# Optimization experiments

Measured on AMD Instinct MI355X. Metric: run time of the kernel, lower is better.

## Reference

```python
import jax, jax.numpy as jnp
import numpy as np

B, DIM, H, W = 4, 96, 256, 256
HEADS = 4
EPS = 1e-12

def conv1x1(x, w, b):
    # x: [b,c,h,w], w: [o,c,1,1], b: [o]
    return jnp.einsum('bchw,oc->bohw', x, w[:, :, 0, 0]) + b[None, :, None, None]

def dwconv3x3(x, w, b):
    # depthwise 3x3, w: [c,1,3,3]
    c = x.shape[1]
    y = jax.lax.conv_general_dilated(
        x, w, window_strides=(1, 1), padding='SAME',
        feature_group_count=c, dimension_numbers=('NCHW', 'OIHW', 'NCHW'))
    return y + b[None, :, None, None]

def setup_inputs() -> dict:
    key = jax.random.key(0)
    ks = jax.random.split(key, 16)
    d = DIM
    s = 0.05
    return {
        'content': jax.random.normal(ks[0], (B, d, H, W), jnp.float32),
        'style': jax.random.normal(ks[1], (B, d, H, W), jnp.float32),
        'temperature': jnp.ones((HEADS, 1, 1), jnp.float32),
        'q_w': jax.random.normal(ks[2], (d, d, 1, 1), jnp.float32) * s,
        'q_b': jax.random.normal(ks[3], (d,), jnp.float32) * s,
        'qd_w': jax.random.normal(ks[4], (d, 1, 3, 3), jnp.float32) * s,
        'qd_b': jax.random.normal(ks[5], (d,), jnp.float32) * s,
        'kv_w': jax.random.normal(ks[6], (3 * d, d, 1, 1), jnp.float32) * s,
        'kv_b': jax.random.normal(ks[7], (3 * d,), jnp.float32) * s,
        'kvd_w': jax.random.normal(ks[8], (3 * d, 1, 3, 3), jnp.float32) * s,
        'kvd_b': jax.random.normal(ks[9], (3 * d,), jnp.float32) * s,
        'ps_w': jax.random.normal(ks[10], (d, d, 1, 1), jnp.float32) * s,
        'ps_b': jax.random.normal(ks[11], (d,), jnp.float32) * s,
        'psh_w': jax.random.normal(ks[12], (d, d, 1, 1), jnp.float32) * s,
        'psh_b': jax.random.normal(ks[13], (d,), jnp.float32) * s,
    }

def _heads(x, b, h, w):
    # [b, head*c, h, w] -> [b, head, c, h*w]
    return x.reshape(b, HEADS, x.shape[1] // HEADS, h * w)

def reference(content, style, temperature, q_w, q_b, qd_w, qd_b,
              kv_w, kv_b, kvd_w, kvd_b, ps_w, ps_b, psh_w, psh_b):
    b, c, h, w = content.shape
    kv = dwconv3x3(conv1x1(style, kv_w, kv_b), kvd_w, kvd_b)
    k, v_scale, v_shift = jnp.split(kv, 3, axis=1)
    q = dwconv3x3(conv1x1(content, q_w, q_b), qd_w, qd_b)

    q = _heads(q, b, h, w)
    k = _heads(k, b, h, w)
    v_scale = _heads(v_scale, b, h, w)
    v_shift = _heads(v_shift, b, h, w)

    # L2-normalize over spatial dim (torch F.normalize eps=1e-12)
    q = q / jnp.maximum(jnp.linalg.norm(q, axis=-1, keepdims=True), EPS)
    k = k / jnp.maximum(jnp.linalg.norm(k, axis=-1, keepdims=True), EPS)

    # attn: [b, head, c, c] (channel attention, tiny)
    attn = jnp.einsum('bhcn,bhdn->bhcd', q, k) * temperature[None]
    attn = jax.nn.softmax(attn, axis=-1)

    scale = jnp.einsum('bhcd,bhdn->bhcn', attn, v_scale).reshape(b, c, h, w)
    shift = jnp.einsum('bhcd,bhdn->bhcn', attn, v_shift).reshape(b, c, h, w)

    scale = conv1x1(scale, ps_w, ps_b)
    shift = conv1x1(shift, psh_w, psh_b)
    return (scale, shift)
```

## Files before the change

kernel.cpp:

```cpp
#include <hip/hip_runtime.h>

#define NB 4
#define C 96
#define HH 256
#define WW 256
#define NPIX (HH*WW)
#define HEADS 4
#define CH 24

#define NTX2 16
#define NTY2 19
#define NTILES (NTX2*NTY2)
#define YP 296
#define QP 264
#define VP 104
#define KSPLIT 128
#define YR 24
#define YC 392
#define XTP 76
#define VCH 40

#define WS_SUMSQ_Q 0
#define WS_SUMSQ_K (WS_SUMSQ_Q + NB*C)
#define WS_GRAM    (WS_SUMSQ_K + NB*C)
#define WS_MS      (WS_GRAM + NB*HEADS*CH*CH)
#define WS_MSH     (WS_MS + NB*C*C)

#define XT_OFF_BYTES ((size_t)335872)
#define XT_BYTES   ((size_t)2*NB*NPIX*96*2)

#define F_PSQ_OFF   (XT_OFF_BYTES + XT_BYTES)
#define F_PSQ_BYTES ((size_t)NTILES*NB*192*4)
#define F_PG_OFF    (F_PSQ_OFF + F_PSQ_BYTES)
#define F_PG_BYTES  ((size_t)NTILES*NB*HEADS*1024*4)
#define F_MB_OFF    (F_PG_OFF + F_PG_BYTES)
#define F_MB_BYTES  ((size_t)2*NB*96*96*2)
#define F_WS_NEED   (F_MB_OFF + F_MB_BYTES)

#define QK_OFF    (XT_OFF_BYTES + XT_BYTES)
#define QK_BYTES  ((size_t)2*NB*96*NPIX*2)
#define PG_OFF    (QK_OFF + QK_BYTES)
#define PG_BYTES  ((size_t)KSPLIT*NB*9216*4)
#define PSQ_OFF   (PG_OFF + PG_BYTES)
#define PSQ_BYTES ((size_t)4*NTILES*NB*48*4)
#define MB_OFF    (PSQ_OFF + PSQ_BYTES)
#define MB_BYTES  ((size_t)2*NB*96*96*2)
#define WB_OFF    (MB_OFF + MB_BYTES)
#define WB_BYTES  ((size_t)384*96*2)
#define WS_NEED3  (WB_OFF + WB_BYTES)

typedef short short8 __attribute__((ext_vector_type(8)));
typedef float f32x4 __attribute__((ext_vector_type(4)));
typedef float f32x16 __attribute__((ext_vector_type(16)));

__device__ __forceinline__ unsigned short f2b(float f){
  unsigned u = __float_as_uint(f);
  unsigned r = u + 0x7FFFu + ((u >> 16) & 1u);
  return (unsigned short)(r >> 16);
}
__device__ __forceinline__ float b2f(unsigned short s){
  return __uint_as_float(((unsigned)s) << 16);
}
__device__ __forceinline__ unsigned cvtpk(float lo, float hi){
  unsigned r;
  asm("v_cvt_pk_bf16_f32 %0, %1, %2" : "=v"(r) : "v"(lo), "v"(hi));
  return r;
}
__device__ __forceinline__ short8 pack8(float4 a, float4 b){
  short8 r;
  r[0]=(short)f2b(a.x); r[1]=(short)f2b(a.y); r[2]=(short)f2b(a.z); r[3]=(short)f2b(a.w);
  r[4]=(short)f2b(b.x); r[5]=(short)f2b(b.y); r[6]=(short)f2b(b.z); r[7]=(short)f2b(b.w);
  return r;
}

__global__ __launch_bounds__(256) void k0t(
  const float* __restrict__ content, const float* __restrict__ style,
  unsigned short* __restrict__ xt, int cm)
{
  __shared__ unsigned short Xt[96*XTP];
  const int t = threadIdx.x;
  const int n0 = blockIdx.x * 64;
  const int b = blockIdx.y, src = blockIdx.z;
  const int gyr = n0 >> 8, gxb = n0 & 255;
  const float* in = (src ? style : content) + (size_t)b*C*NPIX;
  #pragma unroll
  for (int i = 0; i < 6; ++i){
    int s = i*256 + t;
    int r = s >> 4, c4 = s & 15;
    float4 f = *(const float4*)(in + (size_t)r*NPIX + n0 + c4*4);
    unsigned lo = ((unsigned)f2b(f.y) << 16) | f2b(f.x);
    unsigned hi = ((unsigned)f2b(f.w) << 16) | f2b(f.z);
    *(uint2*)&Xt[r*XTP + c4*4] = make_uint2(lo, hi);
  }
  __syncthreads();
  unsigned* dst = (unsigned*)(xt + ((size_t)src*NB + b)*NPIX*96);
  #pragma unroll
  for (int i = 0; i < 12; ++i){
    int s = i*256 + t;
    int j = s / 48, c2 = s - j*48;
    unsigned v = ((unsigned)Xt[(c2*2+1)*XTP + j] << 16) | Xt[(c2*2)*XTP + j];
    size_t np = cm ? ((size_t)(gxb + j)*HH + gyr) : (size_t)(n0 + j);
    dst[np*48 + c2] = v;
  }
}

__global__ __launch_bounds__(256) void kwpack(
  const float* __restrict__ q_w, const float* __restrict__ kv_w,
  unsigned short* __restrict__ wb)
{
  int i = blockIdx.x*256 + threadIdx.x;
  if (i < 9216) wb[i] = f2b(q_w[i]);
  else if (i < 36864) wb[i] = f2b(kv_w[i - 9216]);
}

__global__ __launch_bounds__(512, 4) void kconv(
  const unsigned short* __restrict__ xt, const unsigned short* __restrict__ wb,
  const float* __restrict__ q_b, const float* __restrict__ qd_w, const float* __restrict__ qd_b,
  const float* __restrict__ kv_b, const float* __restrict__ kvd_w, const float* __restrict__ kvd_b,
  unsigned short* __restrict__ qk, float* __restrict__ psq)
{
  __shared__ unsigned short Ysh[48*YC];
  __shared__ float red[48];
  const int t = threadIdx.x, lane = t & 63, w = t >> 6;
  const int tile = blockIdx.x, b = blockIdx.y, z = blockIdx.z;
  const int txx = tile & 15, tyy = tile >> 4;
  const int gx0 = txx*16, gy0 = tyy*14;
  const unsigned short* xsrc = xt + ((size_t)((z < 2 ? 0 : 1)*NB + b))*NPIX*96;
  const int wrow0 = (z < 2) ? z*48 : 96 + (z-2)*48;
  const float* cb  = (z<2) ? q_b  + z*48           : kv_b  + (size_t)(z-2)*48;
  const float* dww = (z<2) ? qd_w + (size_t)z*48*9 : kvd_w + (size_t)(z-2)*48*9;
  const float* dwb = (z<2) ? qd_b + z*48           : kvd_b + (size_t)(z-2)*48;
  unsigned short* dst0 = (z < 2)
      ? qk + ((size_t)(0*NB + b)*96 + (size_t)z*48)*NPIX
      : qk + ((size_t)(1*NB + b)*96 + (size_t)(z-2)*48)*NPIX;

  if (t < 48) red[t] = 0.f;

  const int hy = lane & 15, khalf = lane >> 4;
  const int gyh = gy0 - 1 + hy;
  short8 xf[3][3]; bool imv[3];
  const int np = (w < 2) ? 3 : 2;
  #pragma unroll
  for (int i = 0; i < 3; ++i){
    if (i >= np) break;
    int pt = w + i*8;
    int gx = gx0 - 1 + pt;
    bool im = (gx>=0) && (gx<WW) && (gyh>=0) && (gyh<HH);
    imv[i] = im;
    const unsigned short* xp = xsrc + (size_t)(im ? (gx*HH + gyh) : 0)*96 + khalf*8;
    short8 zz = {};
    #pragma unroll
    for (int kk = 0; kk < 3; ++kk){
      short8 v = *(const short8*)(xp + kk*32);
      xf[i][kk] = im ? v : zz;
    }
  }

  #pragma unroll 1
  for (int mi = 0; mi < 3; ++mi){
    const unsigned short* wp = wb + (size_t)(wrow0 + mi*16 + hy)*96 + khalf*8;
    short8 a0 = *(const short8*)(wp);
    short8 a1 = *(const short8*)(wp + 32);
    short8 a2 = *(const short8*)(wp + 64);
    float4 bv = *(const float4*)&cb[mi*16 + khalf*4];
    #pragma unroll
    for (int i = 0; i < 3; ++i){
      if (i >= np) break;
      int pt = w + i*8;
      f32x4 acc = {bv.x, bv.y, bv.z, bv.w};
      acc = __builtin_amdgcn_mfma_f32_16x16x32_bf16(a0, xf[i][0], acc, 0,0,0);
      acc = __builtin_amdgcn_mfma_f32_16x16x32_bf16(a1, xf[i][1], acc, 0,0,0);
      acc = __builtin_amdgcn_mfma_f32_16x16x32_bf16(a2, xf[i][2], acc, 0,0,0);
      #pragma unroll
      for (int r = 0; r < 4; ++r){
        int ch = mi*16 + khalf*4 + r;
        Ysh[ch*YC + hy*YR + pt] = imv[i] ? f2b(acc[r]) : (unsigned short)0;
      }
    }
  }
  __syncthreads();

  for (int sl = lane; sl < 84; sl += 64){
    int slot = w*84 + sl;
    int c = slot / 14, py = slot - (slot/14)*14;
    int gy = gy0 + py;
    if (gy < HH){
      const float* wd = dww + (size_t)c*9;
      float w00=wd[0],w01=wd[1],w02=wd[2],w10=wd[3],w11=wd[4],w12=wd[5],w20=wd[6],w21=wd[7],w22=wd[8];
      float bb = dwb[c];
      const unsigned short* yb = &Ysh[c*YC + py*YR];
      float o[16];
      #pragma unroll
      for (int half = 0; half < 2; ++half){
        float u[3][10];
        #pragma unroll
        for (int uu = 0; uu < 3; ++uu){
          const unsigned short* rp = yb + uu*YR + half*8;
          short8 s = *(const short8*)rp;
          unsigned ex = *(const unsigned*)(rp + 8);
          #pragma unroll
          for (int j = 0; j < 8; ++j) u[uu][j] = b2f((unsigned short)s[j]);
          u[uu][8] = b2f((unsigned short)(ex & 0xffffu));
          u[uu][9] = b2f((unsigned short)(ex >> 16));
        }
        #pragma unroll
        for (int j = 0; j < 8; ++j){
          float s = bb;
          s = fmaf(w00,u[0][j],s); s = fmaf(w01,u[0][j+1],s); s = fmaf(w02,u[0][j+2],s);
          s = fmaf(w10,u[1][j],s); s = fmaf(w11,u[1][j+1],s); s = fmaf(w12,u[1][j+2],s);
          s = fmaf(w20,u[2][j],s); s = fmaf(w21,u[2][j+1],s); s = fmaf(w22,u[2][j+2],s);
          o[half*8 + j] = s;
        }
      }
      float sq = 0.f;
      #pragma unroll
      for (int j = 0; j < 16; ++j) sq = fmaf(o[j], o[j], sq);
      atomicAdd(&red[c], sq);
      unsigned vvp[8];
      #pragma unroll
      for (int jj = 0; jj < 8; ++jj) vvp[jj] = cvtpk(o[2*jj], o[2*jj+1]);
      unsigned short* qp = dst0 + (size_t)c*NPIX + (size_t)gy*WW + gx0;
      *(uint4*)qp       = make_uint4(vvp[0], vvp[1], vvp[2], vvp[3]);
      *(uint4*)(qp + 8) = make_uint4(vvp[4], vvp[5], vvp[6], vvp[7]);
    }
  }
  __syncthreads();
  if (t < 48)
    psq[((size_t)(z*NTILES + tile)*NB + b)*48 + t] = red[t];
}

__global__ __launch_bounds__(384) void kgram(
  const unsigned short* __restrict__ qk, float* __restrict__ pg)
{
  const int t = threadIdx.x, lane = t & 63, wv = t >> 6;
  const int ks = blockIdx.x, b = blockIdx.y;
  const int n0 = ks * (NPIX / KSPLIT);
  const unsigned short* qb = qk + ((size_t)(0*NB + b)*96)*NPIX;
  const unsigned short* kb = qk + ((size_t)(1*NB + b)*96)*NPIX;
  f32x4 acc[6];
  #pragma unroll
  for (int i = 0; i < 6; ++i) acc[i] = (f32x4){0.f,0.f,0.f,0.f};
  #pragma unroll 1
  for (int st = 0; st < (NPIX/KSPLIT)/32; ++st){
    int off = n0 + st*32 + (lane>>4)*8;
    short8 bf = *(const short8*)(kb + (size_t)(wv*16 + (lane&15))*NPIX + off);
    #pragma unroll
    for (int ci = 0; ci < 6; ++ci){
      short8 af = *(const short8*)(qb + (size_t)(ci*16 + (lane&15))*NPIX + off);
      acc[ci] = __builtin_amdgcn_mfma_f32_16x16x32_bf16(af, bf, acc[ci], 0,0,0);
    }
  }
  float* dst = pg + ((size_t)ks*NB + b)*9216;
  #pragma unroll
  for (int ci = 0; ci < 6; ++ci){
    #pragma unroll
    for (int r = 0; r < 4; ++r)
      dst[(ci*6 + wv)*256 + ((lane>>4)*4 + r)*16 + (lane&15)] = acc[ci][r];
  }
}

__global__ __launch_bounds__(256) void kgredN(
  const float* __restrict__ pg, const float* __restrict__ psq, float* __restrict__ ws)
{
  const int b = blockIdx.x, by = blockIdx.y, t = threadIdx.x;
  if (by < 36){
    int ci = by / 6;
    int qrow = ci*16 + (t >> 4), krow = (by - ci*6)*16 + (t & 15);
    float s = 0.f;
    for (int ks = 0; ks < KSPLIT; ++ks)
      s += pg[((size_t)ks*NB + b)*9216 + by*256 + t];
    int h = qrow / CH;
    if (krow / CH == h)
      ws[WS_GRAM + ((size_t)(b*HEADS + h)*CH + (qrow % CH))*CH + (krow % CH)] = s;
  } else {
    if (t < 192){
      int src = t / 96, c = t - (t/96)*96;
      int zz = src*2 + (c/48), cc = c - (c/48)*48;
      float s = 0.f;
      for (int tile = 0; tile < NTILES; ++tile)
        s += psq[((size_t)(zz*NTILES + tile)*NB + b)*48 + cc];
      ws[(src ? WS_SUMSQ_K : WS_SUMSQ_Q) + b*C + c] = s;
    }
  }
}

__global__ void k2_attn(
  const float* __restrict__ temp,
  const float* __restrict__ ps_w, const float* __restrict__ psh_w,
  float* __restrict__ ws, unsigned short* __restrict__ mb)
{
  const int b = blockIdx.x;
  const int t = threadIdx.x;
  __shared__ float attn[C * CH];
  __shared__ float nq[C], nk[C];
  if (t < C){
    nq[t] = fmaxf(sqrtf(ws[WS_SUMSQ_Q + b * C + t]), 1e-12f);
    nk[t] = fmaxf(sqrtf(ws[WS_SUMSQ_K + b * C + t]), 1e-12f);
  }
  __syncthreads();
  if (t < C){
    int h = t / CH;
    const float* g = ws + WS_GRAM + (((size_t)b * HEADS + h) * CH + (t % CH)) * CH;
    float tp = temp[h];
    float row[CH];
    float mx = -3.4e38f;
    #pragma unroll
    for (int d = 0; d < CH; ++d){
      row[d] = g[d] / (nq[t] * nk[h * CH + d]) * tp;
      mx = fmaxf(mx, row[d]);
    }
    float s = 0.f;
    #pragma unroll
    for (int d = 0; d < CH; ++d){ row[d] = expf(row[d] - mx); s += row[d]; }
    float inv = 1.f / s;
    #pragma unroll
    for (int d = 0; d < CH; ++d) attn[t * CH + d] = row[d] * inv;
  }
  __syncthreads();
  for (int idx = t; idx < C * C; idx += 256){
    int o = idx / C, dg = idx - o * C;
    int h = dg / CH, d = dg - h * CH;
    float s1 = 0.f, s2 = 0.f;
    #pragma unroll
    for (int c2 = 0; c2 < CH; ++c2){
      float a = attn[(h * CH + c2) * CH + d];
      s1 = fmaf(ps_w [(size_t)o * C + h * CH + c2], a, s1);
      s2 = fmaf(psh_w[(size_t)o * C + h * CH + c2], a, s2);
    }
    ws[WS_MS  + (size_t)b * C * C + idx] = s1;
    ws[WS_MSH + (size_t)b * C * C + idx] = s2;
    if (mb){
      mb[((size_t)0*NB + b)*9216 + idx] = f2b(s1);
      mb[((size_t)1*NB + b)*9216 + idx] = f2b(s2);
    }
  }
}

__global__ __launch_bounds__(512, 4) void kvm(
  const unsigned short* __restrict__ xt, const unsigned short* __restrict__ wb,
  const float* __restrict__ kv_b, const float* __restrict__ kvd_w, const float* __restrict__ kvd_b,
  const unsigned short* __restrict__ mb,
  const float* __restrict__ ps_b, const float* __restrict__ psh_b,
  float* __restrict__ out)
{
  __shared__ unsigned short Ysh[32*YC];
  __shared__ unsigned short vS[224*VCH];
  const int t = threadIdx.x, lane = t & 63, w = t >> 6;
  const int tile = blockIdx.x, b = blockIdx.y, z = blockIdx.z;
  const int txx = tile & 15, tyy = tile >> 4;
  const int gx0 = txx*16, gy0 = tyy*14;
  const unsigned short* xsrc = xt + ((size_t)(NB + b))*NPIX*96;

  const int hy = lane & 15, khalf = lane >> 4;
  const int gyh = gy0 - 1 + hy;
  short8 xf[3][3]; bool imv[3];
  const int np = (w < 2) ? 3 : 2;
  #pragma unroll
  for (int i = 0; i < 3; ++i){
    if (i >= np) break;
    int pt = w + i*8;
    int gx = gx0 - 1 + pt;
    bool im = (gx>=0) && (gx<WW) && (gyh>=0) && (gyh<HH);
    imv[i] = im;
    const unsigned short* xp = xsrc + (size_t)(im ? (gx*HH + gyh) : 0)*96 + khalf*8;
    short8 zz = {};
    #pragma unroll
    for (int kk = 0; kk < 3; ++kk){
      short8 v = *(const short8*)(xp + kk*32);
      xf[i][kk] = im ? v : zz;
    }
  }

  const float* bias = z ? psh_b : ps_b;
  f32x4 acc[6][2];
  #pragma unroll
  for (int mi = 0; mi < 6; ++mi){
    float4 bv = *(const float4*)&bias[mi*16 + khalf*4];
    acc[mi][0] = (f32x4){bv.x, bv.y, bv.z, bv.w};
    acc[mi][1] = acc[mi][0];
  }
  const unsigned short* mbp = mb + ((size_t)z*NB + b)*9216;

  #pragma unroll 1
  for (int ck = 0; ck < 3; ++ck){
    const int kvrow0 = 96 + z*96 + ck*32;
    #pragma unroll 1
    for (int mi2 = 0; mi2 < 2; ++mi2){
      const unsigned short* wp = wb + (size_t)(96 + kvrow0 + mi2*16 + hy)*96 + khalf*8;
      short8 a0 = *(const short8*)(wp);
      short8 a1 = *(const short8*)(wp + 32);
      short8 a2 = *(const short8*)(wp + 64);
      float4 bv = *(const float4*)&kv_b[kvrow0 + mi2*16 + khalf*4];
      #pragma unroll
      for (int i = 0; i < 3; ++i){
        if (i >= np) break;
        int pt = w + i*8;
        f32x4 a = {bv.x, bv.y, bv.z, bv.w};
        a = __builtin_amdgcn_mfma_f32_16x16x32_bf16(a0, xf[i][0], a, 0,0,0);
        a = __builtin_amdgcn_mfma_f32_16x16x32_bf16(a1, xf[i][1], a, 0,0,0);
        a = __builtin_amdgcn_mfma_f32_16x16x32_bf16(a2, xf[i][2], a, 0,0,0);
        #pragma unroll
        for (int r = 0; r < 4; ++r){
          int ch = mi2*16 + khalf*4 + r;
          Ysh[ch*YC + hy*YR + pt] = imv[i] ? f2b(a[r]) : (unsigned short)0;
        }
      }
    }
    __syncthreads();
    if (t < 448){
      int c2 = t & 31, py = t >> 5;
      const float* wd = kvd_w + (size_t)(kvrow0 + c2)*9;
      float w00=wd[0],w01=wd[1],w02=wd[2],w10=wd[3],w11=wd[4],w12=wd[5],w20=wd[6],w21=wd[7],w22=wd[8];
      float bb = kvd_b[kvrow0 + c2];
      const unsigned short* yb = &Ysh[c2*YC + py*YR];
      float o[16];
      #pragma unroll
      for (int half = 0; half < 2; ++half){
        float u[3][10];
        #pragma unroll
        for (int uu = 0; uu < 3; ++uu){
          const unsigned short* rp = yb + uu*YR + half*8;
          short8 s = *(const short8*)rp;
          unsigned ex = *(const unsigned*)(rp + 8);
          #pragma unroll
          for (int j = 0; j < 8; ++j) u[uu][j] = b2f((unsigned short)s[j]);
          u[uu][8] = b2f((unsigned short)(ex & 0xffffu));
          u[uu][9] = b2f((unsigned short)(ex >> 16));
        }
        #pragma unroll
        for (int j = 0; j < 8; ++j){
          float s = bb;
          s = fmaf(w00,u[0][j],s); s = fmaf(w01,u[0][j+1],s); s = fmaf(w02,u[0][j+2],s);
          s = fmaf(w10,u[1][j],s); s = fmaf(w11,u[1][j+1],s); s = fmaf(w12,u[1][j+2],s);
          s = fmaf(w20,u[2][j],s); s = fmaf(w21,u[2][j+1],s); s = fmaf(w22,u[2][j+2],s);
          o[half*8 + j] = s;
        }
      }
      #pragma unroll
      for (int jj = 0; jj < 8; ++jj){
        unsigned p = cvtpk(o[2*jj], o[2*jj+1]);
        vS[(py*16 + 2*jj    )*VCH + c2] = (unsigned short)p;
        vS[(py*16 + 2*jj + 1)*VCH + c2] = (unsigned short)(p >> 16);
      }
    }
    __syncthreads();
    #pragma unroll
    for (int mi = 0; mi < 6; ++mi){
      short8 a = *(const short8*)(mbp + (size_t)(mi*16 + hy)*96 + ck*32 + khalf*8);
      #pragma unroll
      for (int gi = 0; gi < 2; ++gi){
        int g = w + gi*8;
        if (g < 14){
          short8 bf = *(const short8*)&vS[(size_t)(g*16 + hy)*VCH + khalf*8];
          acc[mi][gi] = __builtin_amdgcn_mfma_f32_16x16x32_bf16(a, bf, acc[mi][gi], 0,0,0);
        }
      }
    }
    __syncthreads();
  }

  float* ob = out + ((size_t)z*NB + b)*(size_t)C*NPIX;
  #pragma unroll
  for (int gi = 0; gi < 2; ++gi){
    int g = w + gi*8;
    int gy = gy0 + g;
    if (g < 14 && gy < HH){
      #pragma unroll
      for (int mi = 0; mi < 6; ++mi){
        #pragma unroll
        for (int r = 0; r < 4; ++r)
          __builtin_nontemporal_store(acc[mi][gi][r],
            &ob[(size_t)(mi*16 + khalf*4 + r)*NPIX + (size_t)gy*WW + gx0 + hy]);
      }
    }
  }
}

__device__ __forceinline__ void conv48c(
  const unsigned short* __restrict__ xbase, const float* __restrict__ wmat,
  const float* __restrict__ bias, int row0,
  int gx0, int gy0, int lane, int w, unsigned short* __restrict__ Ysh)
{
  const int hy = lane & 15, khalf = lane >> 4;
  const int gy = gy0 - 1 + hy;
  short8 xf[3][3]; bool imv[3]; int np = (w < 2) ? 3 : 2;
  #pragma unroll
  for (int i = 0; i < 3; ++i){
    if (i >= np) break;
    int pt = w + i*8;
    int gx = gx0 - 1 + pt;
    bool im = (gx>=0) && (gx<WW) && (gy>=0) && (gy<HH);
    imv[i] = im;
    int n = im ? (gy*WW + gx) : 0;
    const unsigned short* xp = xbase + (size_t)n*96 + khalf*8;
    short8 z = {};
    #pragma unroll
    for (int kk = 0; kk < 3; ++kk){
      short8 v = *(const short8*)(xp + kk*32);
      xf[i][kk] = im ? v : z;
    }
  }
  #pragma unroll 1
  for (int mi = 0; mi < 3; ++mi){
    int orow = row0 + mi*16 + hy;
    const float* wp = wmat + (size_t)orow*96 + khalf*8;
    short8 a0 = pack8(*(const float4*)(wp),    *(const float4*)(wp+4));
    short8 a1 = pack8(*(const float4*)(wp+32), *(const float4*)(wp+36));
    short8 a2 = pack8(*(const float4*)(wp+64), *(const float4*)(wp+68));
    float4 bv = *(const float4*)&bias[row0 + mi*16 + khalf*4];
    #pragma unroll
    for (int i = 0; i < 3; ++i){
      if (i >= np) break;
      int pt = w + i*8;
      f32x4 acc = {bv.x, bv.y, bv.z, bv.w};
      acc = __builtin_amdgcn_mfma_f32_16x16x32_bf16(a0, xf[i][0], acc, 0,0,0);
      acc = __builtin_amdgcn_mfma_f32_16x16x32_bf16(a1, xf[i][1], acc, 0,0,0);
      acc = __builtin_amdgcn_mfma_f32_16x16x32_bf16(a2, xf[i][2], acc, 0,0,0);
      #pragma unroll
      for (int r = 0; r < 4; ++r){
        int ch = mi*16 + khalf*4 + r;
        Ysh[ch*YP + pt*16 + hy] = imv[i] ? f2b(acc[r]) : (unsigned short)0;
      }
    }
  }
}

__global__ __launch_bounds__(512, 4) void kqk(
  const unsigned short* __restrict__ xt,
  const float* __restrict__ q_w, const float* __restrict__ q_b,
  const float* __restrict__ qd_w, const float* __restrict__ qd_b,
  const float* __restrict__ kv_w, const float* __restrict__ kv_b,
  const float* __restrict__ kvd_w, const float* __restrict__ kvd_b,
  float* __restrict__ pg, float* __restrict__ psq)
{
  __shared__ unsigned short Ysh[48*YP];
  __shared__ unsigned short qS[48*QP];
  __shared__ unsigned short kT[48*QP];
  __shared__ float redq[C], redk[C];

  const int t = threadIdx.x, lane = t & 63, w = t >> 6;
  const int b = blockIdx.y, tile = blockIdx.x;
  const int txx = tile & 15, tyy = tile >> 4;
  const int gx0 = txx*16, gy0 = tyy*14;
  if (t < C){ redq[t] = 0.f; redk[t] = 0.f; }
  __syncthreads();

  const unsigned short* xc = xt + ((size_t)(0*NB + b))*NPIX*96;
  const unsigned short* xs = xt + ((size_t)(1*NB + b))*NPIX*96;

  auto dwQK = [&](const float* dww, const float* dwb, int wrow0,
                  unsigned short* dst, float* red){
    for (int slot = t; slot < 48*16; slot += 512){
      int c = slot >> 4, j = slot & 15;
      const unsigned short* yb = &Ysh[c*YP + j*16];
      float u0[16], u1[16], u2[16];
      {
        short8 s0 = *(const short8*)(yb);
        short8 s1 = *(const short8*)(yb+8);
        short8 s2 = *(const short8*)(yb+16), s3 = *(const short8*)(yb+24);
        short8 s4 = *(const short8*)(yb+32), s5 = *(const short8*)(yb+40);
        #pragma unroll
        for (int u = 0; u < 8; ++u){
          u0[u]=b2f((unsigned short)s0[u]); u0[u+8]=b2f((unsigned short)s1[u]);
          u1[u]=b2f((unsigned short)s2[u]); u1[u+8]=b2f((unsigned short)s3[u]);
          u2[u]=b2f((unsigned short)s4[u]); u2[u+8]=b2f((unsigned short)s5[u]);
        }
      }
      const float* wd = dww + (size_t)(wrow0 + c)*9;
      float w00=wd[0],w01=wd[1],w02=wd[2],w10=wd[3],w11=wd[4],w12=wd[5],w20=wd[6],w21=wd[7],w22=wd[8];
      float bb = dwb[wrow0 + c];
      unsigned short vv[16];
      float sq = 0.f;
      #pragma unroll
      for (int py = 0; py < 14; ++py){
        float s = bb;
        s = fmaf(w00,u0[py],s); s = fmaf(w10,u0[py+1],s); s = fmaf(w20,u0[py+2],s);
        s = fmaf(w01,u1[py],s); s = fmaf(w11,u1[py+1],s); s = fmaf(w21,u1[py+2],s);
        s = fmaf(w02,u2[py],s); s = fmaf(w12,u2[py+1],s); s = fmaf(w22,u2[py+2],s);
        if (gy0 + py >= HH) s = 0.f;
        sq = fmaf(s, s, sq);
        vv[py] = f2b(s);
      }
      vv[14] = 0; vv[15] = 0;
      atomicAdd(&red[wrow0 + c], sq);
      *(short8*)&dst[c*QP + j*16]     = *(short8*)&vv[0];
      *(short8*)&dst[c*QP + j*16 + 8] = *(short8*)&vv[8];
    }
  };

  auto gram = [&](int cc){
    int hl = w & 1, slice = w >> 1;
    int cl = lane & 31; bool cv = cl < CH;
    int row = hl*CH + (cv ? cl : 0);
    f32x16 g;
    #pragma unroll
    for (int r = 0; r < 16; ++r) g[r] = 0.f;
    short8 z = {};
    for (int ks = slice; ks < 16; ks += 4){
      int ko = ks*16 + (lane>>5)*8;
      short8 qa = *(const short8*)&qS[row*QP + ko];
      short8 kb = *(const short8*)&kT[row*QP + ko];
      if (!cv){ qa = z; kb = z; }
      g = __builtin_amdgcn_mfma_f32_32x32x16_bf16(qa, kb, g, 0,0,0);
    }
    float* stg = (float*)Ysh;
    if (slice != 0){
      float* dst = stg + (size_t)(hl*3 + slice - 1)*1024;
      #pragma unroll
      for (int r = 0; r < 16; ++r) dst[r*64 + lane] = g[r];
    }
    __syncthreads();
    if (slice == 0){
      const float* s0 = stg + (size_t)(hl*3 + 0)*1024;
      const float* s1 = stg + (size_t)(hl*3 + 1)*1024;
      const float* s2 = stg + (size_t)(hl*3 + 2)*1024;
      float* dst = pg + ((size_t)(tile*NB + b)*HEADS + cc*2 + hl)*1024;
      #pragma unroll
      for (int r = 0; r < 16; ++r){
        int ix = r*64 + lane;
        dst[ix] = g[r] + s0[ix] + s1[ix] + s2[ix];
      }
    }
  };

  #pragma unroll 1
  for (int cc = 0; cc < 2; ++cc){
    conv48c(xc, q_w, q_b, cc*48, gx0, gy0, lane, w, Ysh);
    __syncthreads();
    dwQK(qd_w, qd_b, cc*48, qS, redq);
    __syncthreads();
    conv48c(xs, kv_w, kv_b, cc*48, gx0, gy0, lane, w, Ysh);
    __syncthreads();
    dwQK(kvd_w, kvd_b, cc*48, kT, redk);
    __syncthreads();
    gram(cc);
    __syncthreads();
  }
  if (t < 192){
    float v = (t < 96) ? redq[t] : redk[t - 96];
    psq[(size_t)(tile*NB + b)*192 + t] = v;
  }
}

__global__ __launch_bounds__(256) void kgredF(
  const float* __restrict__ pg, const float* __restrict__ psq, float* __restrict__ ws)
{
  const int bh = blockIdx.x;
  const int b = bh >> 2, h = bh & 3;
  const int t = threadIdx.x;
  float a0=0.f, a1=0.f, a2=0.f, a3=0.f, sq=0.f;
  for (int tile = 0; tile < NTILES; ++tile){
    const float* p = pg + ((size_t)(tile*NB + b)*HEADS + h)*1024;
    a0 += p[t]; a1 += p[t+256]; a2 += p[t+512]; a3 += p[t+768];
    if (t < 48){
      int ch = h*CH + (t % CH);
      sq += psq[(size_t)(tile*NB + b)*192 + (t < CH ? ch : 96 + ch)];
    }
  }
  if (t < 48){
    if (t < CH) ws[WS_SUMSQ_Q + b*C + h*CH + t] = sq;
    else        ws[WS_SUMSQ_K + b*C + h*CH + (t - CH)] = sq;
  }
  float accs[4] = {a0, a1, a2, a3};
  #pragma unroll
  for (int i = 0; i < 4; ++i){
    int idx = i*256 + t;
    int r = idx >> 6, ln = idx & 63;
    int row = (r&3) + 8*(r>>2) + 4*(ln>>5);
    int col = ln & 31;
    if (row < CH && col < CH)
      ws[WS_GRAM + ((size_t)(b*HEADS + h)*CH + row)*CH + col] = accs[i];
  }
}

__global__ __launch_bounds__(512, 4) void kv_out(
  const unsigned short* __restrict__ xs,
  const float* __restrict__ kv_w, const float* __restrict__ kv_b,
  const float* __restrict__ kvd_w, const float* __restrict__ kvd_b,
  const float* __restrict__ ps_b, const float* __restrict__ psh_b,
  const unsigned short* __restrict__ mb, float* __restrict__ out)
{
  __shared__ unsigned short Ysh[48*YP];
  __shared__ unsigned short vS2[224*VP];
  const int t = threadIdx.x, lane = t & 63, w = t >> 6;
  const int b = blockIdx.y, tile = blockIdx.x;
  const int txx = tile & 15, tyy = tile >> 4;
  const int gx0 = txx*16, gy0 = tyy*14;
  const unsigned short* xb_ = xs + (size_t)b*NPIX*96;

  #pragma unroll 1
  for (int which = 0; which < 2; ++which){
    #pragma unroll 1
    for (int cv = 0; cv < 2; ++cv){
      int row0 = 96 + which*96 + cv*48;
      conv48c(xb_, kv_w, kv_b, row0, gx0, gy0, lane, w, Ysh);
      __syncthreads();
      for (int slot = t; slot < 48*16; slot += 512){
        int c = slot >> 4, j = slot & 15;
        const unsigned short* yb = &Ysh[c*YP + j*16];
        float u0[16], u1[16], u2[16];
        {
          short8 s0 = *(const short8*)(yb),    s1 = *(const short8*)(yb+8);
          short8 s2 = *(const short8*)(yb+16), s3 = *(const short8*)(yb+24);
          short8 s4 = *(const short8*)(yb+32), s5 = *(const short8*)(yb+40);
          #pragma unroll
          for (int u = 0; u < 8; ++u){
            u0[u]=b2f((unsigned short)s0[u]); u0[u+8]=b2f((unsigned short)s1[u]);
            u1[u]=b2f((unsigned short)s2[u]); u1[u+8]=b2f((unsigned short)s3[u]);
            u2[u]=b2f((unsigned short)s4[u]); u2[u+8]=b2f((unsigned short)s5[u]);
          }
        }
        const float* wd = kvd_w + (size_t)(row0 + c)*9;
        float w00=wd[0],w01=wd[1],w02=wd[2],w10=wd[3],w11=wd[4],w12=wd[5],w20=wd[6],w21=wd[7],w22=wd[8];
        float bb = kvd_b[row0 + c];
        #pragma unroll
        for (int py = 0; py < 14; ++py){
          float s = bb;
          s = fmaf(w00,u0[py],s); s = fmaf(w10,u0[py+1],s); s = fmaf(w20,u0[py+2],s);
          s = fmaf(w01,u1[py],s); s = fmaf(w11,u1[py+1],s); s = fmaf(w21,u1[py+2],s);
          s = fmaf(w02,u2[py],s); s = fmaf(w12,u2[py+1],s); s = fmaf(w22,u2[py+2],s);
          vS2[(py*16 + j)*VP + cv*48 + c] = f2b(s);
        }
      }
      __syncthreads();
    }
    const unsigned short* mbp = mb + ((size_t)which*NB + b)*9216;
    const float* bias = which ? psh_b : ps_b;
    float* ob = out + (size_t)which*NB*C*NPIX + (size_t)b*C*NPIX;
    for (int tl = w; tl < 84; tl += 8){
      int mi = tl / 14, n = tl - mi*14;
      const unsigned short* mp = mbp + (size_t)(mi*16 + (lane&15))*96 + (lane>>4)*8;
      short8 a0 = *(const short8*)(mp);
      short8 a1 = *(const short8*)(mp + 32);
      short8 a2 = *(const short8*)(mp + 64);
      float4 bv = *(const float4*)&bias[mi*16 + (lane>>4)*4];
      f32x4 acc = {bv.x, bv.y, bv.z, bv.w};
      const unsigned short* xb = &vS2[(size_t)(n*16 + (lane&15))*VP + (lane>>4)*8];
      acc = __builtin_amdgcn_mfma_f32_16x16x32_bf16(a0, *(const short8*)(xb),    acc, 0,0,0);
      acc = __builtin_amdgcn_mfma_f32_16x16x32_bf16(a1, *(const short8*)(xb+32), acc, 0,0,0);
      acc = __builtin_amdgcn_mfma_f32_16x16x32_bf16(a2, *(const short8*)(xb+64), acc, 0,0,0);
      int gy = gy0 + n;
      if (gy < HH){
        #pragma unroll
        for (int r = 0; r < 4; ++r)
          ob[(size_t)(mi*16 + (lane>>4)*4 + r)*NPIX + gy*WW + gx0 + (lane&15)] = acc[r];
      }
    }
    __syncthreads();
  }
}

extern "C" void kernel_launch(void* const* d_in, const int* in_sizes, int n_in,
                              void* d_out, int out_size, void* d_ws, size_t ws_size,
                              hipStream_t stream)
{
  const float* content = (const float*)d_in[0];
  const float* style   = (const float*)d_in[1];
  const float* temp    = (const float*)d_in[2];
  const float* q_w   = (const float*)d_in[3];
  const float* q_b   = (const float*)d_in[4];
  const float* qd_w  = (const float*)d_in[5];
  const float* qd_b  = (const float*)d_in[6];
  const float* kv_w  = (const float*)d_in[7];
  const float* kv_b  = (const float*)d_in[8];
  const float* kvd_w = (const float*)d_in[9];
  const float* kvd_b = (const float*)d_in[10];
  const float* ps_w  = (const float*)d_in[11];
  const float* ps_b  = (const float*)d_in[12];
  const float* psh_w = (const float*)d_in[13];
  const float* psh_b = (const float*)d_in[14];
  float* out = (float*)d_out;
  float* ws  = (float*)d_ws;

  unsigned short* xt = (unsigned short*)((char*)d_ws + XT_OFF_BYTES);

  if (ws_size >= WS_NEED3){
    unsigned short* qk  = (unsigned short*)((char*)d_ws + QK_OFF);
    float* pg  = (float*)((char*)d_ws + PG_OFF);
    float* psq = (float*)((char*)d_ws + PSQ_OFF);
    unsigned short* mb = (unsigned short*)((char*)d_ws + MB_OFF);
    unsigned short* wb = (unsigned short*)((char*)d_ws + WB_OFF);

    k0t<<<dim3(NPIX/64, NB, 2), dim3(256), 0, stream>>>(content, style, xt, 1);
    kwpack<<<dim3(144), dim3(256), 0, stream>>>(q_w, kv_w, wb);
    kconv<<<dim3(NTILES, NB, 4), dim3(512), 0, stream>>>(
        xt, wb, q_b, qd_w, qd_b, kv_b, kvd_w, kvd_b, qk, psq);
    kgram<<<dim3(KSPLIT, NB), dim3(384), 0, stream>>>(qk, pg);
    kgredN<<<dim3(NB, 37), dim3(256), 0, stream>>>(pg, psq, ws);
    k2_attn<<<dim3(NB), dim3(256), 0, stream>>>(temp, ps_w, psh_w, ws, mb);
    kvm<<<dim3(NTILES, NB, 2), dim3(512), 0, stream>>>(
        xt, wb, kv_b, kvd_w, kvd_b, mb, ps_b, psh_b, out);
  } else {
    float* pg  = (float*)((char*)d_ws + F_PG_OFF);
    float* psq = (float*)((char*)d_ws + F_PSQ_OFF);
    unsigned short* mb = (unsigned short*)((char*)d_ws + F_MB_OFF);
    k0t<<<dim3(NPIX/64, NB, 2), dim3(256), 0, stream>>>(content, style, xt, 0);
    kqk<<<dim3(NTILES, NB), dim3(512), 0, stream>>>(
        xt, q_w, q_b, qd_w, qd_b, kv_w, kv_b, kvd_w, kvd_b, pg, psq);
    kgredF<<<dim3(NB*HEADS), dim3(256), 0, stream>>>(pg, psq, ws);
    k2_attn<<<dim3(NB), dim3(256), 0, stream>>>(temp, ps_w, psh_w, ws, mb);
    kv_out<<<dim3(NTILES, NB), dim3(512), 0, stream>>>(
        xt + (size_t)NB*NPIX*96, kv_w, kv_b, kvd_w, kvd_b, ps_b, psh_b, mb, out);
  }
}
```

Baseline: 405.1 us.

## Retile kvm kernel to 32x8 pixel tiles with flattened halo mapping

Changes the kvm output tile from 16x14 to 32x8 pixels, which gives exactly 256 tiles with no partial tiles or idle waves. The 34x10 halo is now flattened across the waves' MFMA positions. The depthwise stage uses all 512 threads and each wave writes one full 32-wide output row, removing the g<14 guards. The trade-offs are a larger halo per pixel (340 vs 288) and extra integer division for halo indexing.

```diff
diff --git a/kernel.cpp b/kernel.cpp
--- a/kernel.cpp
+++ b/kernel.cpp
@@ -19,6 +19,11 @@
 #define YC 392
 #define XTP 76
 #define VCH 40
+
+#define VHP2 340
+#define VXP2 40
+#define VYC2 400
+#define NTV2 256
 
 #define WS_SUMSQ_Q 0
 #define WS_SUMSQ_K (WS_SUMSQ_Q + NB*C)
@@ -343,26 +348,26 @@
   const float* __restrict__ ps_b, const float* __restrict__ psh_b,
   float* __restrict__ out)
 {
-  __shared__ unsigned short Ysh[32*YC];
-  __shared__ unsigned short vS[224*VCH];
+  __shared__ unsigned short Ysh[32*VYC2];
+  __shared__ unsigned short vS[256*VCH];
   const int t = threadIdx.x, lane = t & 63, w = t >> 6;
   const int tile = blockIdx.x, b = blockIdx.y, z = blockIdx.z;
-  const int txx = tile & 15, tyy = tile >> 4;
-  const int gx0 = txx*16, gy0 = tyy*14;
+  const int gx0 = (tile & 7)*32, gy0 = (tile >> 3)*8;
   const unsigned short* xsrc = xt + ((size_t)(NB + b))*NPIX*96;
 
-  const int hy = lane & 15, khalf = lane >> 4;
-  const int gyh = gy0 - 1 + hy;
-  short8 xf[3][3]; bool imv[3];
-  const int np = (w < 2) ? 3 : 2;
+  const int pos = lane & 15, khalf = lane >> 4;
+  const int npv = (w < 6) ? 3 : 2;
+  short8 xf[3][3]; bool imv[3]; int hxv[3], hyv[3];
   #pragma unroll
   for (int i = 0; i < 3; ++i){
-    if (i >= np) break;
-    int pt = w + i*8;
-    int gx = gx0 - 1 + pt;
-    bool im = (gx>=0) && (gx<WW) && (gyh>=0) && (gyh<HH);
+    if (i >= npv) break;
+    int hp = (w + i*8)*16 + pos;
+    int hx = hp / 10, hyy = hp - hx*10;
+    hxv[i] = hx; hyv[i] = hyy;
+    int gx = gx0 - 1 + hx, gy = gy0 - 1 + hyy;
+    bool im = (hp < VHP2) && (gx>=0) && (gx<WW) && (gy>=0) && (gy<HH);
     imv[i] = im;
-    const unsigned short* xp = xsrc + (size_t)(im ? (gx*HH + gyh) : 0)*96 + khalf*8;
+    const unsigned short* xp = xsrc + (size_t)(im ? (gx*HH + gy) : 0)*96 + khalf*8;
     short8 zz = {};
     #pragma unroll
     for (int kk = 0; kk < 3; ++kk){
@@ -386,15 +391,14 @@
     const int kvrow0 = 96 + z*96 + ck*32;
     #pragma unroll 1
     for (int mi2 = 0; mi2 < 2; ++mi2){
-      const unsigned short* wp = wb + (size_t)(96 + kvrow0 + mi2*16 + hy)*96 + khalf*8;
+      const unsigned short* wp = wb + (size_t)(96 + kvrow0 + mi2*16 + pos)*96 + khalf*8;
       short8 a0 = *(const short8*)(wp);
       short8 a1 = *(const short8*)(wp + 32);
       short8 a2 = *(const short8*)(wp + 64);
       float4 bv = *(const float4*)&kv_b[kvrow0 + mi2*16 + khalf*4];
       #pragma unroll
       for (int i = 0; i < 3; ++i){
-        if (i >= np) break;
-        int pt = w + i*8;
+        if (i >= npv) break;
         f32x4 a = {bv.x, bv.y, bv.z, bv.w};
         a = __builtin_amdgcn_mfma_f32_16x16x32_bf16(a0, xf[i][0], a, 0,0,0);
         a = __builtin_amdgcn_mfma_f32_16x16x32_bf16(a1, xf[i][1], a, 0,0,0);
@@ -402,24 +406,23 @@
         #pragma unroll
         for (int r = 0; r < 4; ++r){
           int ch = mi2*16 + khalf*4 + r;
-          Ysh[ch*YC + hy*YR + pt] = imv[i] ? f2b(a[r]) : (unsigned short)0;
+          Ysh[ch*VYC2 + hyv[i]*VXP2 + hxv[i]] = imv[i] ? f2b(a[r]) : (unsigned short)0;
         }
       }
     }
     __syncthreads();
-    if (t < 448){
-      int c2 = t & 31, py = t >> 5;
+    {
+      int c2 = t >> 4, py = (t >> 1) & 7, xh = t & 1;
       const float* wd = kvd_w + (size_t)(kvrow0 + c2)*9;
       float w00=wd[0],w01=wd[1],w02=wd[2],w10=wd[3],w11=wd[4],w12=wd[5],w20=wd[6],w21=wd[7],w22=wd[8];
       float bb = kvd_b[kvrow0 + c2];
-      const unsigned short* yb = &Ysh[c2*YC + py*YR];
       float o[16];
       #pragma unroll
       for (int half = 0; half < 2; ++half){
         float u[3][10];
         #pragma unroll
         for (int uu = 0; uu < 3; ++uu){
-          const unsigned short* rp = yb + uu*YR + half*8;
+          const unsigned short* rp = &Ysh[c2*VYC2 + (py+uu)*VXP2 + xh*16 + half*8];
           short8 s = *(const short8*)rp;
           unsigned ex = *(const unsigned*)(rp + 8);
           #pragma unroll
@@ -436,42 +439,37 @@
           o[half*8 + j] = s;
         }
       }
+      int pb = py*32 + xh*16;
       #pragma unroll
       for (int jj = 0; jj < 8; ++jj){
         unsigned p = cvtpk(o[2*jj], o[2*jj+1]);
-        vS[(py*16 + 2*jj    )*VCH + c2] = (unsigned short)p;
-        vS[(py*16 + 2*jj + 1)*VCH + c2] = (unsigned short)(p >> 16);
+        vS[(pb + 2*jj    )*VCH + c2] = (unsigned short)p;
+        vS[(pb + 2*jj + 1)*VCH + c2] = (unsigned short)(p >> 16);
       }
     }
     __syncthreads();
     #pragma unroll
     for (int mi = 0; mi < 6; ++mi){
-      short8 a = *(const short8*)(mbp + (size_t)(mi*16 + hy)*96 + ck*32 + khalf*8);
+      short8 a = *(const short8*)(mbp + (size_t)(mi*16 + pos)*96 + ck*32 + khalf*8);
       #pragma unroll
       for (int gi = 0; gi < 2; ++gi){
-        int g = w + gi*8;
-        if (g < 14){
-          short8 bf = *(const short8*)&vS[(size_t)(g*16 + hy)*VCH + khalf*8];
-          acc[mi][gi] = __builtin_amdgcn_mfma_f32_16x16x32_bf16(a, bf, acc[mi][gi], 0,0,0);
-        }
+        int g = 2*w + gi;
+        short8 bf = *(const short8*)&vS[(size_t)(g*16 + pos)*VCH + khalf*8];
+        acc[mi][gi] = __builtin_amdgcn_mfma_f32_16x16x32_bf16(a, bf, acc[mi][gi], 0,0,0);
       }
     }
     __syncthreads();
   }
 
   float* ob = out + ((size_t)z*NB + b)*(size_t)C*NPIX;
-  #pragma unroll
-  for (int gi = 0; gi < 2; ++gi){
-    int g = w + gi*8;
-    int gy = gy0 + g;
-    if (g < 14 && gy < HH){
-      #pragma unroll
-      for (int mi = 0; mi < 6; ++mi){
-        #pragma unroll
-        for (int r = 0; r < 4; ++r)
-          __builtin_nontemporal_store(acc[mi][gi][r],
-            &ob[(size_t)(mi*16 + khalf*4 + r)*NPIX + (size_t)gy*WW + gx0 + hy]);
-      }
+  const int gy = gy0 + w;
+  #pragma unroll
+  for (int mi = 0; mi < 6; ++mi){
+    #pragma unroll
+    for (int r = 0; r < 4; ++r){
+      float* base = &ob[(size_t)(mi*16 + khalf*4 + r)*NPIX + (size_t)gy*WW + gx0 + pos];
+      __builtin_nontemporal_store(acc[mi][0][r], base);
+      __builtin_nontemporal_store(acc[mi][1][r], base + 16);
     }
   }
 }
@@ -788,7 +786,7 @@
     kgram<<<dim3(KSPLIT, NB), dim3(384), 0, stream>>>(qk, pg);
     kgredN<<<dim3(NB, 37), dim3(256), 0, stream>>>(pg, psq, ws);
     k2_attn<<<dim3(NB), dim3(256), 0, stream>>>(temp, ps_w, psh_w, ws, mb);
-    kvm<<<dim3(NTILES, NB, 2), dim3(512), 0, stream>>>(
+    kvm<<<dim3(NTV2, NB, 2), dim3(512), 0, stream>>>(
         xt, wb, kv_b, kvd_w, kvd_b, mb, ps_b, psh_b, out);
   } else {
     float* pg  = (float*)((char*)d_ws + F_PG_OFF);
```

After: 409.9 us. Within noise of the previous version (+1.2%).
